# Kernel tuning notes

Measured on AMD Instinct MI355X. Metric: run time of the kernel, lower is better.

Reference implementation:

```python
import jax, jax.numpy as jnp
import numpy as np

E = 256
H_HEADS = 8
HD = E // H_HEADS
NEG = -1e9


def setup_inputs() -> dict:
    key = jax.random.key(0)
    ks = jax.random.split(key, 16)
    B, Q, Hh, Ww = 16, 100, 64, 64
    S = Hh * Ww
    std = 1.0 / np.sqrt(E)
    inp = {
        "query_features": jax.random.normal(ks[0], (B, Q, E), jnp.float32),
        "image_features": jax.random.normal(ks[1], (B, E, Hh, Ww), jnp.float32),
        "mask": jax.random.randint(ks[2], (B, Q, Hh, Ww), 0, 2) > 0,
        "pos_query_embeddings": jax.random.normal(ks[3], (B, Q, E), jnp.float32),
        "pos_image_embeddings": jax.random.normal(ks[4], (B, S, E), jnp.float32),
        "Wq": jax.random.normal(ks[5], (E, E), jnp.float32) * std,
        "bq": jnp.zeros((E,), jnp.float32),
        "Wk": jax.random.normal(ks[6], (E, E), jnp.float32) * std,
        "bk": jnp.zeros((E,), jnp.float32),
        "Wv": jax.random.normal(ks[7], (E, E), jnp.float32) * std,
        "bv": jnp.zeros((E,), jnp.float32),
        "Wo": jax.random.normal(ks[8], (E, E), jnp.float32) * std,
        "bo": jnp.zeros((E,), jnp.float32),
    }
    return inp


def reference(query_features, image_features, mask, pos_query_embeddings,
              pos_image_embeddings, Wq, bq, Wk, bk, Wv, bv, Wo, bo):
    B, _, Hh, Ww = image_features.shape
    Q = query_features.shape[1]
    S = Hh * Ww
    # (B, S, E)
    img = jnp.transpose(image_features.reshape(B, E, S), (0, 2, 1))
    q = (query_features + pos_query_embeddings) @ Wq.T + bq  # (B,Q,E)
    k = (img + pos_image_embeddings) @ Wk.T + bk              # (B,S,E)
    v = img @ Wv.T + bv                                       # (B,S,E)
    q = q.reshape(B, Q, H_HEADS, HD).transpose(0, 2, 1, 3)    # (B,H,Q,D)
    k = k.reshape(B, S, H_HEADS, HD).transpose(0, 2, 1, 3)    # (B,H,S,D)
    v = v.reshape(B, S, H_HEADS, HD).transpose(0, 2, 1, 3)
    scale = 1.0 / jnp.sqrt(jnp.asarray(HD, q.dtype))
    scores = jnp.einsum('bhqd,bhsd->bhqs', q, k) * scale
    amask = mask.reshape(B, 1, Q, S)
    scores = jnp.where(amask, scores, NEG)
    attn = jax.nn.softmax(scores, axis=-1)
    out = jnp.einsum('bhqs,bhsd->bhqd', attn, v)
    out = out.transpose(0, 2, 1, 3).reshape(B, Q, E)
    return out @ Wo.T + bo
```

## Files before the change

kernel.cpp:

```cpp
#include <hip/hip_runtime.h>
#include <math.h>

#define BB 16
#define QQ 100
#define EE 256
#define NH 8
#define HD 32
#define SS 4096
#define QP 128
#define NZ 8
#define SCHUNK (SS / NZ)
#define M0 8.0f

typedef _Float16 half8_t __attribute__((ext_vector_type(8)));
typedef _Float16 half4_t __attribute__((ext_vector_type(4)));
typedef float floatx4 __attribute__((ext_vector_type(4)));

__global__ __launch_bounds__(256) void cvt_kernel(
    const float* __restrict__ img,
    const float* __restrict__ pos,
    _Float16* __restrict__ aK16, _Float16* __restrict__ aV16)
{
    const int b  = blockIdx.z;
    const int f0 = blockIdx.y * 64;
    const int s0 = blockIdx.x * 64;
    const int t  = threadIdx.x;

    __shared__ float T[64][65];

    const float* imgb = img + (size_t)b * EE * SS;
    #pragma unroll
    for (int p = 0; p < 4; ++p) {
        int idx = t + p * 256;
        int fl = idx >> 4;
        int s4 = idx & 15;
        float4 v = *(const float4*)&imgb[(size_t)(f0 + fl) * SS + s0 + s4 * 4];
        T[fl][s4 * 4 + 0] = v.x;
        T[fl][s4 * 4 + 1] = v.y;
        T[fl][s4 * 4 + 2] = v.z;
        T[fl][s4 * 4 + 3] = v.w;
    }
    __syncthreads();

    #pragma unroll
    for (int p = 0; p < 2; ++p) {
        int idx = t + p * 256;
        int f8 = idx & 7;
        int s  = idx >> 3;
        size_t rowbase = ((size_t)(b * SS + s0 + s)) * EE + f0;
        float4 p0 = *(const float4*)&pos[rowbase + f8 * 8];
        float4 p1 = *(const float4*)&pos[rowbase + f8 * 8 + 4];
        float pv[8] = {p0.x, p0.y, p0.z, p0.w, p1.x, p1.y, p1.z, p1.w};
        _Float16 hv[8], hk[8];
        #pragma unroll
        for (int j = 0; j < 8; ++j) {
            float iv = T[f8 * 8 + j][s];
            hv[j] = (_Float16)iv;
            hk[j] = (_Float16)(iv + pv[j]);
        }
        *(uint4*)(aV16 + rowbase + f8 * 8) = *(const uint4*)&hv[0];
        *(uint4*)(aK16 + rowbase + f8 * 8) = *(const uint4*)&hk[0];
    }
}

__global__ __launch_bounds__(256) void wcvt_kernel(
    const float* __restrict__ Wk, const float* __restrict__ Wv,
    _Float16* __restrict__ wk16, _Float16* __restrict__ wv16)
{
    int gid = blockIdx.x * 256 + threadIdx.x;
    int idx = gid * 4;
    const float* src; _Float16* dst; int li;
    if (idx < EE * EE) { src = Wk; dst = wk16; li = idx; }
    else               { src = Wv; dst = wv16; li = idx - EE * EE; }
    float4 v = *(const float4*)(src + li);
    half4_t h; h[0] = (_Float16)v.x; h[1] = (_Float16)v.y;
    h[2] = (_Float16)v.z; h[3] = (_Float16)v.w;
    *(half4_t*)(dst + li) = h;
}

__global__ __launch_bounds__(256) void maskpack_kernel(
    const int* __restrict__ mask, unsigned* __restrict__ mbits)
{
    int gid  = blockIdx.x * 256 + threadIdx.x;
    int lane = gid & 63;
    int F    = gid & ~63;
    int s    = (F & (SS - 1)) + lane;
    int qp   = (F >> 12) & (QP - 1);
    int b    = F >> 19;
    int qc   = min(qp, QQ - 1);
    int v    = mask[((size_t)(b * QQ + qc)) * SS + s];
    unsigned long long bal = __ballot(v != 0);
    int w = (F & (SS - 1)) >> 5;
    if (lane == 0)
        mbits[((size_t)(b * (SS / 32) + w)) * QP + qp] = (unsigned)bal;
    if (lane == 32)
        mbits[((size_t)(b * (SS / 32) + w + 1)) * QP + qp] = (unsigned)(bal >> 32);
}

__device__ inline void gl_lds16(const _Float16* g, _Float16* l) {
    __builtin_amdgcn_global_load_lds(
        (const __attribute__((address_space(1))) void*)g,
        (__attribute__((address_space(3))) void*)l, 16, 0, 0);
}

__global__ __launch_bounds__(256) void gemm_bt_f16(
    const _Float16* __restrict__ A,
    const _Float16* __restrict__ W,
    const float*    __restrict__ bias,
    _Float16* __restrict__ out, int vt_mode)
{
    __shared__ _Float16 smem[128 * 72];
    _Float16* As = smem;
    _Float16* Bs = smem + 128 * 32;

    const int t = threadIdx.x;
    const int w = t >> 6, l = t & 63;
    const int gg = l >> 4, li = l & 15;
    const int row0 = blockIdx.x * 128;
    const int e0   = blockIdx.y * 128;
    const int wm = w & 1, wn = w >> 1;

    const int ldrow = l >> 2;
    const int ldcol = (l & 3) * 8;

    floatx4 acc[4][4] = {};

    for (int f0 = 0; f0 < EE; f0 += 32) {
        #pragma unroll
        for (int r = 0; r < 2; ++r) {
            int rb = r * 64 + w * 16;
            int arow = rb + ldrow;
            gl_lds16(A + (size_t)(row0 + arow) * EE + f0 + ldcol, &As[rb * 32]);
            gl_lds16(W + (size_t)(e0 + arow) * EE + f0 + ldcol,   &Bs[rb * 32]);
        }
        __syncthreads();

        half8_t af[4], bf[4];
        #pragma unroll
        for (int i = 0; i < 4; ++i) {
            int m = wm * 64 + i * 16 + li;
            af[i] = *(const half8_t*)&As[m * 32 + gg * 8];
            int n = wn * 64 + i * 16 + li;
            bf[i] = *(const half8_t*)&Bs[n * 32 + gg * 8];
        }
        #pragma unroll
        for (int i = 0; i < 4; ++i)
            #pragma unroll
            for (int j = 0; j < 4; ++j)
                acc[i][j] = __builtin_amdgcn_mfma_f32_16x16x32_f16(
                    af[i], bf[j], acc[i][j], 0, 0, 0);
        __syncthreads();
    }

    if (!vt_mode) {
        #pragma unroll
        for (int j = 0; j < 4; ++j) {
            int e = e0 + wn * 64 + j * 16 + li;
            float bj = bias[e];
            #pragma unroll
            for (int i = 0; i < 4; ++i) {
                int srow = row0 + wm * 64 + i * 16 + gg * 4;
                #pragma unroll
                for (int r = 0; r < 4; ++r)
                    out[(size_t)(srow + r) * EE + e] = (_Float16)(acc[i][j][r] + bj);
            }
        }
    } else {
        const int bq = row0 >> 12;
        const int m0 = row0 & 4095;
        #pragma unroll
        for (int p = 0; p < 2; ++p) {
            if (wm == p) {
                #pragma unroll
                for (int j = 0; j < 4; ++j) {
                    int e_loc = wn * 64 + j * 16 + li;
                    float bj = bias[e0 + e_loc];
                    #pragma unroll
                    for (int i = 0; i < 4; ++i) {
                        int s_loc = i * 16 + gg * 4;
                        half4_t h4;
                        #pragma unroll
                        for (int r = 0; r < 4; ++r)
                            h4[r] = (_Float16)(acc[i][j][r] + bj);
                        *(half4_t*)&smem[e_loc * 72 + s_loc] = h4;
                    }
                }
            }
            __syncthreads();
            #pragma unroll
            for (int sw = 0; sw < 4; ++sw) {
                int row = sw * 32 + (t >> 3);
                int e = e0 + row;
                int hh = e >> 5, dd = e & 31;
                half8_t v8 = *(const half8_t*)&smem[row * 72 + (t & 7) * 8];
                *(half8_t*)(out + ((size_t)((bq * NH + hh) * HD + dd)) * SS
                            + m0 + p * 64 + (t & 7) * 8) = v8;
            }
            __syncthreads();
        }
    }
}

__global__ __launch_bounds__(256) void proj_kernel(
    const float* __restrict__ x1, const float* __restrict__ x2,
    const float* __restrict__ W, const float* __restrict__ bias,
    float* __restrict__ outf, _Float16* __restrict__ out16,
    float oscale, int has_x2)
{
    const int row0 = blockIdx.x * 8;
    const int t = threadIdx.x;
    __shared__ float xs[8][256];

    #pragma unroll
    for (int p = 0; p < 8; ++p) {
        int idx = t + p * 256;
        int f = idx & 255, j = idx >> 8;
        size_t g = (size_t)(row0 + j) * EE + f;
        float v = x1[g];
        if (has_x2) v += x2[g];
        xs[j][f] = v;
    }
    __syncthreads();

    const int e = t;
    const float* wrow = W + (size_t)e * EE;
    float acc[8];
    const float bv = bias[e];
    #pragma unroll
    for (int j = 0; j < 8; ++j) acc[j] = bv;

    #pragma unroll 4
    for (int f4 = 0; f4 < 64; ++f4) {
        float4 w4 = *(const float4*)(wrow + f4 * 4);
        #pragma unroll
        for (int j = 0; j < 8; ++j) {
            float4 x4 = *(const float4*)&xs[j][f4 * 4];
            acc[j] = fmaf(w4.x, x4.x, acc[j]);
            acc[j] = fmaf(w4.y, x4.y, acc[j]);
            acc[j] = fmaf(w4.z, x4.z, acc[j]);
            acc[j] = fmaf(w4.w, x4.w, acc[j]);
        }
    }
    if (out16) {
        #pragma unroll
        for (int j = 0; j < 8; ++j)
            out16[(size_t)(row0 + j) * EE + e] = (_Float16)(acc[j] * oscale);
    } else {
        #pragma unroll
        for (int j = 0; j < 8; ++j)
            outf[(size_t)(row0 + j) * EE + e] = acc[j];
    }
}

__global__ __launch_bounds__(256) void attn_mfma_kernel(
    const _Float16* __restrict__ q16,
    const _Float16* __restrict__ kbuf,
    const _Float16* __restrict__ vt,
    const unsigned* __restrict__ mbits,
    float* __restrict__ part,
    float* __restrict__ pl)
{
    const int z = blockIdx.x, h = blockIdx.y, b = blockIdx.z;
    const int t = threadIdx.x;
    const int w = t >> 6, l = t & 63;
    const int g = l >> 4, li = l & 15;

    __shared__ _Float16 ks[64 * 40];
    __shared__ _Float16 vs[32 * 72];
    __shared__ _Float16 ps[128 * 72];
    __shared__ unsigned mw[2][QP];

    half8_t qf[2];
    {
        int q0r = min(32 * w + li, QQ - 1);
        int q1r = min(32 * w + 16 + li, QQ - 1);
        qf[0] = *(const half8_t*)(q16 + ((size_t)(b * QQ + q0r)) * EE + h * HD + g * 8);
        qf[1] = *(const half8_t*)(q16 + ((size_t)(b * QQ + q1r)) * EE + h * HD + g * 8);
    }

    float lsum[2][4] = {{0.f}};
    floatx4 accO[2][2] = {};

    for (int it = 0; it < SCHUNK / 64; ++it) {
        const int sblk = z * SCHUNK + it * 64;

        {
            int sl = t >> 2, koff = (t & 3) * 8;
            *(half8_t*)&ks[sl * 40 + koff] =
                *(const half8_t*)(kbuf + ((size_t)(b * SS + sblk + sl)) * EE + h * HD + koff);
            int dl = t >> 3, soff = (t & 7) * 8;
            *(half8_t*)&vs[dl * 72 + soff] =
                *(const half8_t*)(vt + ((size_t)((b * NH + h) * HD + dl)) * SS + sblk + soff);
            mw[t >> 7][t & 127] =
                mbits[((size_t)(b * (SS / 32) + (sblk >> 5) + (t >> 7))) * QP + (t & 127)];
        }
        __syncthreads();

        half8_t kf[4];
        #pragma unroll
        for (int st = 0; st < 4; ++st)
            kf[st] = *(const half8_t*)&ks[(st * 16 + li) * 40 + g * 8];
        floatx4 sc[2][4];
        #pragma unroll
        for (int qt = 0; qt < 2; ++qt)
            #pragma unroll
            for (int st = 0; st < 4; ++st) {
                floatx4 zero = {0.f, 0.f, 0.f, 0.f};
                sc[qt][st] = __builtin_amdgcn_mfma_f32_16x16x32_f16(
                    qf[qt], kf[st], zero, 0, 0, 0);
            }

        #pragma unroll
        for (int qt = 0; qt < 2; ++qt) {
            int qrow0 = 32 * w + qt * 16 + 4 * g;
            unsigned w0r[4], w1r[4];
            #pragma unroll
            for (int r = 0; r < 4; ++r) {
                w0r[r] = mw[0][qrow0 + r];
                w1r[r] = mw[1][qrow0 + r];
            }
            #pragma unroll
            for (int st = 0; st < 4; ++st)
                #pragma unroll
                for (int r = 0; r < 4; ++r) {
                    unsigned word = (st < 2) ? w0r[r] : w1r[r];
                    int keep = (word >> ((st & 1) * 16 + li)) & 1;
                    float pv = keep ? __expf(sc[qt][st][r] - M0) : 0.f;
                    _Float16 ph = (_Float16)pv;
                    lsum[qt][r] += (float)ph;
                    ps[(qrow0 + r) * 72 + st * 16 + li] = ph;
                }
        }

        half8_t vb[2][2];
        #pragma unroll
        for (int dt = 0; dt < 2; ++dt) {
            vb[dt][0] = *(const half8_t*)&vs[(dt * 16 + li) * 72 + g * 8];
            vb[dt][1] = *(const half8_t*)&vs[(dt * 16 + li) * 72 + 32 + g * 8];
        }
        #pragma unroll
        for (int qt = 0; qt < 2; ++qt) {
            half8_t a0 = *(const half8_t*)&ps[(32 * w + qt * 16 + li) * 72 + g * 8];
            half8_t a1 = *(const half8_t*)&ps[(32 * w + qt * 16 + li) * 72 + 32 + g * 8];
            #pragma unroll
            for (int dt = 0; dt < 2; ++dt) {
                accO[qt][dt] = __builtin_amdgcn_mfma_f32_16x16x32_f16(
                    a0, vb[dt][0], accO[qt][dt], 0, 0, 0);
                accO[qt][dt] = __builtin_amdgcn_mfma_f32_16x16x32_f16(
                    a1, vb[dt][1], accO[qt][dt], 0, 0, 0);
            }
        }
        __syncthreads();
    }

    #pragma unroll
    for (int qt = 0; qt < 2; ++qt)
        #pragma unroll
        for (int r = 0; r < 4; ++r) {
            float v = lsum[qt][r];
            v += __shfl_xor(v, 1, 64);
            v += __shfl_xor(v, 2, 64);
            v += __shfl_xor(v, 4, 64);
            v += __shfl_xor(v, 8, 64);
            lsum[qt][r] = v;
        }

    const size_t pbase = (((size_t)z * BB + b) * NH + h) * QP;
    #pragma unroll
    for (int qt = 0; qt < 2; ++qt) {
        int qrow0 = 32 * w + qt * 16 + 4 * g;
        #pragma unroll
        for (int r = 0; r < 4; ++r) {
            int qp = qrow0 + r;
            #pragma unroll
            for (int dt = 0; dt < 2; ++dt)
                part[(pbase + qp) * HD + dt * 16 + li] = accO[qt][dt][r];
            if (li == 0) pl[pbase + qp] = lsum[qt][r];
        }
    }
}

__global__ __launch_bounds__(256) void combine_kernel(
    const float* __restrict__ part, const float* __restrict__ pl,
    float* __restrict__ abuf)
{
    int tid = blockIdx.x * 256 + threadIdx.x;
    int d  = tid & 31;
    int qp = (tid >> 5) & 127;
    int h  = (tid >> 12) & 7;
    int b  = tid >> 15;
    if (qp >= QQ) return;
    float L = 0.f, O = 0.f;
    #pragma unroll
    for (int zz = 0; zz < NZ; ++zz) {
        size_t idx = (((size_t)zz * BB + b) * NH + h) * QP + qp;
        L += pl[idx];
        O += part[idx * HD + d];
    }
    abuf[((size_t)(b * QQ + qp)) * EE + h * HD + d] = O / fmaxf(L, 1e-30f);
}

extern "C" void kernel_launch(void* const* d_in, const int* in_sizes, int n_in,
                              void* d_out, int out_size, void* d_ws, size_t ws_size,
                              hipStream_t stream)
{
    const float* qf   = (const float*)d_in[0];
    const float* img  = (const float*)d_in[1];
    const int*   mask = (const int*)  d_in[2];
    const float* pq   = (const float*)d_in[3];
    const float* pimg = (const float*)d_in[4];
    const float* Wq   = (const float*)d_in[5];
    const float* bq   = (const float*)d_in[6];
    const float* Wk   = (const float*)d_in[7];
    const float* bk   = (const float*)d_in[8];
    const float* Wv   = (const float*)d_in[9];
    const float* bv   = (const float*)d_in[10];
    const float* Wo   = (const float*)d_in[11];
    const float* bo   = (const float*)d_in[12];
    float* out = (float*)d_out;

    const size_t MSE = (size_t)BB * SS * EE;

    _Float16* aK16 = (_Float16*)d_ws;
    _Float16* aV16 = aK16 + MSE;
    _Float16* vtb  = aV16 + MSE;
    _Float16* wk16 = vtb + MSE;
    _Float16* wv16 = wk16 + EE * EE;
    _Float16* q16  = wv16 + EE * EE;
    unsigned* mbits = (unsigned*)(q16 + (size_t)BB * QQ * EE);

    float* part = (float*)aK16;
    float* pl   = part + (size_t)NZ * BB * NH * QP * HD;
    float* abuf = pl + (size_t)NZ * BB * NH * QP;

    const float scale = 0.17677669529663687f;

    cvt_kernel<<<dim3(SS / 64, EE / 64, BB), 256, 0, stream>>>(img, pimg, aK16, aV16);
    wcvt_kernel<<<128, 256, 0, stream>>>(Wk, Wv, wk16, wv16);
    maskpack_kernel<<<(BB * QP * SS) / 256, 256, 0, stream>>>(mask, mbits);
    proj_kernel<<<BB * QQ / 8, 256, 0, stream>>>(qf, pq, Wq, bq, nullptr, q16, scale, 1);
    gemm_bt_f16<<<dim3(BB * SS / 128, EE / 128), 256, 0, stream>>>(aV16, wv16, bv, vtb, 1);
    _Float16* kbuf = aV16;
    gemm_bt_f16<<<dim3(BB * SS / 128, EE / 128), 256, 0, stream>>>(aK16, wk16, bk, kbuf, 0);
    attn_mfma_kernel<<<dim3(NZ, NH, BB), 256, 0, stream>>>(q16, kbuf, vtb, mbits, part, pl);
    combine_kernel<<<(BB * NH * QP * HD) / 256, 256, 0, stream>>>(part, pl, abuf);
    proj_kernel<<<BB * QQ / 8, 256, 0, stream>>>(abuf, nullptr, Wo, bo, out, nullptr, 1.f, 0);
}
```

Baseline: 334.2 us.

## Fuse image/weight fp16 conversion with K and V projection GEMMs

Replaces the separate conversion kernels and two fp16 GEMMs with a single kernel. It reads fp32 image and positional features, converts them in registers, and computes both K and V projections for a 64-row tile, writing K row-major and V transposed. This removes the round-trip of the fp16 intermediate activations through global memory and three kernel launches. In exchange, each block re-reads and re-converts the full fp32 Wk/Wv on every K-step. The image loads are strided per thread, and the workspace layout moves the partial buffers so they no longer alias K.

```diff
diff --git a/kernel.cpp b/kernel.cpp
--- a/kernel.cpp
+++ b/kernel.cpp
@@ -15,68 +15,6 @@
 typedef _Float16 half8_t __attribute__((ext_vector_type(8)));
 typedef _Float16 half4_t __attribute__((ext_vector_type(4)));
 typedef float floatx4 __attribute__((ext_vector_type(4)));
-
-__global__ __launch_bounds__(256) void cvt_kernel(
-    const float* __restrict__ img,
-    const float* __restrict__ pos,
-    _Float16* __restrict__ aK16, _Float16* __restrict__ aV16)
-{
-    const int b  = blockIdx.z;
-    const int f0 = blockIdx.y * 64;
-    const int s0 = blockIdx.x * 64;
-    const int t  = threadIdx.x;
-
-    __shared__ float T[64][65];
-
-    const float* imgb = img + (size_t)b * EE * SS;
-    #pragma unroll
-    for (int p = 0; p < 4; ++p) {
-        int idx = t + p * 256;
-        int fl = idx >> 4;
-        int s4 = idx & 15;
-        float4 v = *(const float4*)&imgb[(size_t)(f0 + fl) * SS + s0 + s4 * 4];
-        T[fl][s4 * 4 + 0] = v.x;
-        T[fl][s4 * 4 + 1] = v.y;
-        T[fl][s4 * 4 + 2] = v.z;
-        T[fl][s4 * 4 + 3] = v.w;
-    }
-    __syncthreads();
-
-    #pragma unroll
-    for (int p = 0; p < 2; ++p) {
-        int idx = t + p * 256;
-        int f8 = idx & 7;
-        int s  = idx >> 3;
-        size_t rowbase = ((size_t)(b * SS + s0 + s)) * EE + f0;
-        float4 p0 = *(const float4*)&pos[rowbase + f8 * 8];
-        float4 p1 = *(const float4*)&pos[rowbase + f8 * 8 + 4];
-        float pv[8] = {p0.x, p0.y, p0.z, p0.w, p1.x, p1.y, p1.z, p1.w};
-        _Float16 hv[8], hk[8];
-        #pragma unroll
-        for (int j = 0; j < 8; ++j) {
-            float iv = T[f8 * 8 + j][s];
-            hv[j] = (_Float16)iv;
-            hk[j] = (_Float16)(iv + pv[j]);
-        }
-        *(uint4*)(aV16 + rowbase + f8 * 8) = *(const uint4*)&hv[0];
-        *(uint4*)(aK16 + rowbase + f8 * 8) = *(const uint4*)&hk[0];
-    }
-}
-
-__global__ __launch_bounds__(256) void wcvt_kernel(
-    const float* __restrict__ Wk, const float* __restrict__ Wv,
-    _Float16* __restrict__ wk16, _Float16* __restrict__ wv16)
-{
-    int gid = blockIdx.x * 256 + threadIdx.x;
-    int idx = gid * 4;
-    const float* src; _Float16* dst; int li;
-    if (idx < EE * EE) { src = Wk; dst = wk16; li = idx; }
-    else               { src = Wv; dst = wv16; li = idx - EE * EE; }
-    float4 v = *(const float4*)(src + li);
-    half4_t h; h[0] = (_Float16)v.x; h[1] = (_Float16)v.y;
-    h[2] = (_Float16)v.z; h[3] = (_Float16)v.w;
-    *(half4_t*)(dst + li) = h;
-}
 
 __global__ __launch_bounds__(256) void maskpack_kernel(
     const int* __restrict__ mask, unsigned* __restrict__ mbits)
@@ -97,107 +35,156 @@
         mbits[((size_t)(b * (SS / 32) + w + 1)) * QP + qp] = (unsigned)(bal >> 32);
 }
 
-__device__ inline void gl_lds16(const _Float16* g, _Float16* l) {
-    __builtin_amdgcn_global_load_lds(
-        (const __attribute__((address_space(1))) void*)g,
-        (__attribute__((address_space(3))) void*)l, 16, 0, 0);
-}
-
-__global__ __launch_bounds__(256) void gemm_bt_f16(
-    const _Float16* __restrict__ A,
-    const _Float16* __restrict__ W,
-    const float*    __restrict__ bias,
-    _Float16* __restrict__ out, int vt_mode)
-{
-    __shared__ _Float16 smem[128 * 72];
-    _Float16* As = smem;
-    _Float16* Bs = smem + 128 * 32;
-
-    const int t = threadIdx.x;
-    const int w = t >> 6, l = t & 63;
+__global__ __launch_bounds__(256, 2) void fused_kv_kernel(
+    const float* __restrict__ img,
+    const float* __restrict__ pos,
+    const float* __restrict__ Wk, const float* __restrict__ bk,
+    const float* __restrict__ Wv, const float* __restrict__ bv,
+    _Float16* __restrict__ kbuf,
+    _Float16* __restrict__ vt)
+{
+    __shared__ _Float16 smem[2 * 64 * 40 + 2 * 256 * 40];
+    _Float16* Ak = smem;
+    _Float16* Av = Ak + 64 * 40;
+    _Float16* Bk = Av + 64 * 40;
+    _Float16* Bv = Bk + 256 * 40;
+
+    const int t  = threadIdx.x;
+    const int w  = t >> 6;
+    const int l  = t & 63;
     const int gg = l >> 4, li = l & 15;
-    const int row0 = blockIdx.x * 128;
-    const int e0   = blockIdx.y * 128;
-    const int wm = w & 1, wn = w >> 1;
-
-    const int ldrow = l >> 2;
-    const int ldcol = (l & 3) * 8;
-
-    floatx4 acc[4][4] = {};
-
-    for (int f0 = 0; f0 < EE; f0 += 32) {
-        #pragma unroll
-        for (int r = 0; r < 2; ++r) {
-            int rb = r * 64 + w * 16;
-            int arow = rb + ldrow;
-            gl_lds16(A + (size_t)(row0 + arow) * EE + f0 + ldcol, &As[rb * 32]);
-            gl_lds16(W + (size_t)(e0 + arow) * EE + f0 + ldcol,   &Bs[rb * 32]);
+
+    const int m0 = blockIdx.x * 64;
+    const int b  = m0 >> 12;
+    const int s0 = m0 & (SS - 1);
+
+    const float* imgb = img + (size_t)b * EE * SS + s0;
+    const float* posb = pos + ((size_t)b * SS + s0) * EE;
+
+    const int sf8 = t & 3;
+    const int ss  = t >> 2;
+
+    floatx4 acck[4][4] = {};
+    floatx4 accv[4][4] = {};
+
+    float iv[8], pv[8];
+    {
+        const float* ic = imgb + (size_t)(sf8 * 8) * SS + ss;
+        #pragma unroll
+        for (int j = 0; j < 8; ++j) iv[j] = ic[(size_t)j * SS];
+        float4 p0 = *(const float4*)(posb + (size_t)ss * EE + sf8 * 8);
+        float4 p1 = *(const float4*)(posb + (size_t)ss * EE + sf8 * 8 + 4);
+        pv[0]=p0.x; pv[1]=p0.y; pv[2]=p0.z; pv[3]=p0.w;
+        pv[4]=p1.x; pv[5]=p1.y; pv[6]=p1.z; pv[7]=p1.w;
+    }
+
+    #pragma unroll 1
+    for (int kk = 0; kk < 8; ++kk) {
+        const int f0 = kk * 32;
+        {
+            half8_t hv, hk;
+            #pragma unroll
+            for (int j = 0; j < 8; ++j) {
+                hv[j] = (_Float16)iv[j];
+                hk[j] = (_Float16)(iv[j] + pv[j]);
+            }
+            *(half8_t*)&Av[ss * 40 + sf8 * 8] = hv;
+            *(half8_t*)&Ak[ss * 40 + sf8 * 8] = hk;
+        }
+        #pragma unroll
+        for (int c = 0; c < 8; ++c) {
+            int r = (c & 3) * 64 + (t >> 2);
+            const float* src = ((c < 4) ? Wk : Wv) + (size_t)r * EE + f0 + sf8 * 8;
+            float4 a0 = *(const float4*)src;
+            float4 a1 = *(const float4*)(src + 4);
+            half8_t hw;
+            hw[0]=(_Float16)a0.x; hw[1]=(_Float16)a0.y;
+            hw[2]=(_Float16)a0.z; hw[3]=(_Float16)a0.w;
+            hw[4]=(_Float16)a1.x; hw[5]=(_Float16)a1.y;
+            hw[6]=(_Float16)a1.z; hw[7]=(_Float16)a1.w;
+            _Float16* dst = (c < 4) ? Bk : Bv;
+            *(half8_t*)&dst[r * 40 + sf8 * 8] = hw;
         }
         __syncthreads();
 
-        half8_t af[4], bf[4];
+        if (kk < 7) {
+            const int f1 = f0 + 32;
+            const float* ic = imgb + (size_t)(f1 + sf8 * 8) * SS + ss;
+            #pragma unroll
+            for (int j = 0; j < 8; ++j) iv[j] = ic[(size_t)j * SS];
+            float4 p0 = *(const float4*)(posb + (size_t)ss * EE + f1 + sf8 * 8);
+            float4 p1 = *(const float4*)(posb + (size_t)ss * EE + f1 + sf8 * 8 + 4);
+            pv[0]=p0.x; pv[1]=p0.y; pv[2]=p0.z; pv[3]=p0.w;
+            pv[4]=p1.x; pv[5]=p1.y; pv[6]=p1.z; pv[7]=p1.w;
+        }
+
+        {
+            half8_t af[4], bf[4];
+            #pragma unroll
+            for (int i = 0; i < 4; ++i) {
+                af[i] = *(const half8_t*)&Ak[(i * 16 + li) * 40 + gg * 8];
+                bf[i] = *(const half8_t*)&Bk[(w * 64 + i * 16 + li) * 40 + gg * 8];
+            }
+            #pragma unroll
+            for (int i = 0; i < 4; ++i)
+                #pragma unroll
+                for (int j = 0; j < 4; ++j)
+                    acck[i][j] = __builtin_amdgcn_mfma_f32_16x16x32_f16(
+                        af[i], bf[j], acck[i][j], 0, 0, 0);
+        }
+        {
+            half8_t af[4], bf[4];
+            #pragma unroll
+            for (int i = 0; i < 4; ++i) {
+                af[i] = *(const half8_t*)&Av[(i * 16 + li) * 40 + gg * 8];
+                bf[i] = *(const half8_t*)&Bv[(w * 64 + i * 16 + li) * 40 + gg * 8];
+            }
+            #pragma unroll
+            for (int i = 0; i < 4; ++i)
+                #pragma unroll
+                for (int j = 0; j < 4; ++j)
+                    accv[i][j] = __builtin_amdgcn_mfma_f32_16x16x32_f16(
+                        af[i], bf[j], accv[i][j], 0, 0, 0);
+        }
+        __syncthreads();
+    }
+
+    #pragma unroll
+    for (int j = 0; j < 4; ++j) {
+        int e = w * 64 + j * 16 + li;
+        float bj = bk[e];
         #pragma unroll
         for (int i = 0; i < 4; ++i) {
-            int m = wm * 64 + i * 16 + li;
-            af[i] = *(const half8_t*)&As[m * 32 + gg * 8];
-            int n = wn * 64 + i * 16 + li;
-            bf[i] = *(const half8_t*)&Bs[n * 32 + gg * 8];
-        }
-        #pragma unroll
-        for (int i = 0; i < 4; ++i)
-            #pragma unroll
-            for (int j = 0; j < 4; ++j)
-                acc[i][j] = __builtin_amdgcn_mfma_f32_16x16x32_f16(
-                    af[i], bf[j], acc[i][j], 0, 0, 0);
-        __syncthreads();
-    }
-
-    if (!vt_mode) {
-        #pragma unroll
-        for (int j = 0; j < 4; ++j) {
-            int e = e0 + wn * 64 + j * 16 + li;
-            float bj = bias[e];
-            #pragma unroll
-            for (int i = 0; i < 4; ++i) {
-                int srow = row0 + wm * 64 + i * 16 + gg * 4;
-                #pragma unroll
-                for (int r = 0; r < 4; ++r)
-                    out[(size_t)(srow + r) * EE + e] = (_Float16)(acc[i][j][r] + bj);
-            }
-        }
-    } else {
-        const int bq = row0 >> 12;
-        const int m0 = row0 & 4095;
-        #pragma unroll
-        for (int p = 0; p < 2; ++p) {
-            if (wm == p) {
-                #pragma unroll
-                for (int j = 0; j < 4; ++j) {
-                    int e_loc = wn * 64 + j * 16 + li;
-                    float bj = bias[e0 + e_loc];
-                    #pragma unroll
-                    for (int i = 0; i < 4; ++i) {
-                        int s_loc = i * 16 + gg * 4;
-                        half4_t h4;
-                        #pragma unroll
-                        for (int r = 0; r < 4; ++r)
-                            h4[r] = (_Float16)(acc[i][j][r] + bj);
-                        *(half4_t*)&smem[e_loc * 72 + s_loc] = h4;
-                    }
-                }
-            }
-            __syncthreads();
-            #pragma unroll
-            for (int sw = 0; sw < 4; ++sw) {
-                int row = sw * 32 + (t >> 3);
-                int e = e0 + row;
-                int hh = e >> 5, dd = e & 31;
-                half8_t v8 = *(const half8_t*)&smem[row * 72 + (t & 7) * 8];
-                *(half8_t*)(out + ((size_t)((bq * NH + hh) * HD + dd)) * SS
-                            + m0 + p * 64 + (t & 7) * 8) = v8;
-            }
-            __syncthreads();
-        }
+            int row = m0 + i * 16 + gg * 4;
+            #pragma unroll
+            for (int r = 0; r < 4; ++r)
+                kbuf[(size_t)(row + r) * EE + e] = (_Float16)(acck[i][j][r] + bj);
+        }
+    }
+
+    _Float16* vstage = smem;
+    #pragma unroll
+    for (int j = 0; j < 4; ++j) {
+        int e_loc = w * 64 + j * 16 + li;
+        float bj = bv[e_loc];
+        #pragma unroll
+        for (int i = 0; i < 4; ++i) {
+            int s_loc = i * 16 + gg * 4;
+            half4_t h4;
+            #pragma unroll
+            for (int r = 0; r < 4; ++r)
+                h4[r] = (_Float16)(accv[i][j][r] + bj);
+            *(half4_t*)&vstage[e_loc * 72 + s_loc] = h4;
+        }
+    }
+    __syncthreads();
+    #pragma unroll
+    for (int c = 0; c < 8; ++c) {
+        int row = c * 32 + (t >> 3);
+        int so  = (t & 7) * 8;
+        half8_t v8 = *(const half8_t*)&vstage[row * 72 + so];
+        int hh = row >> 5, dd = row & 31;
+        *(half8_t*)(vt + ((size_t)((b * NH + hh) * HD + dd)) * SS + s0 + so) = v8;
     }
 }
 
@@ -421,27 +408,19 @@
 
     const size_t MSE = (size_t)BB * SS * EE;
 
-    _Float16* aK16 = (_Float16*)d_ws;
-    _Float16* aV16 = aK16 + MSE;
-    _Float16* vtb  = aV16 + MSE;
-    _Float16* wk16 = vtb + MSE;
-    _Float16* wv16 = wk16 + EE * EE;
-    _Float16* q16  = wv16 + EE * EE;
+    _Float16* kbuf = (_Float16*)d_ws;
+    _Float16* vtb  = kbuf + MSE;
+    _Float16* q16  = vtb + MSE;
     unsigned* mbits = (unsigned*)(q16 + (size_t)BB * QQ * EE);
-
-    float* part = (float*)aK16;
+    float* part = (float*)(mbits + (size_t)BB * (SS / 32) * QP);
     float* pl   = part + (size_t)NZ * BB * NH * QP * HD;
     float* abuf = pl + (size_t)NZ * BB * NH * QP;
 
     const float scale = 0.17677669529663687f;
 
-    cvt_kernel<<<dim3(SS / 64, EE / 64, BB), 256, 0, stream>>>(img, pimg, aK16, aV16);
-    wcvt_kernel<<<128, 256, 0, stream>>>(Wk, Wv, wk16, wv16);
     maskpack_kernel<<<(BB * QP * SS) / 256, 256, 0, stream>>>(mask, mbits);
     proj_kernel<<<BB * QQ / 8, 256, 0, stream>>>(qf, pq, Wq, bq, nullptr, q16, scale, 1);
-    gemm_bt_f16<<<dim3(BB * SS / 128, EE / 128), 256, 0, stream>>>(aV16, wv16, bv, vtb, 1);
-    _Float16* kbuf = aV16;
-    gemm_bt_f16<<<dim3(BB * SS / 128, EE / 128), 256, 0, stream>>>(aK16, wk16, bk, kbuf, 0);
+    fused_kv_kernel<<<BB * SS / 64, 256, 0, stream>>>(img, pimg, Wk, bk, Wv, bv, kbuf, vtb);
     attn_mfma_kernel<<<dim3(NZ, NH, BB), 256, 0, stream>>>(q16, kbuf, vtb, mbits, part, pl);
     combine_kernel<<<(BB * NH * QP * HD) / 256, 256, 0, stream>>>(part, pl, abuf);
     proj_kernel<<<BB * QQ / 8, 256, 0, stream>>>(abuf, nullptr, Wo, bo, out, nullptr, 1.f, 0);
```

New measurement: 310.9 us. -7.0%, faster.
